# Kernel optimization log

Hardware: AMD Instinct MI355X
Metric: run time of the kernel (lower is better)

Reference implementation:

```python
import jax, jax.numpy as jnp
import numpy as np

T_Q, T_K, B, H, V = 32, 48, 64, 1024, 32320
MASK_FILL = -65504.0  # GNMT uses fp16 min


def setup_inputs() -> dict:
    key = jax.random.key(0)
    ks = jax.random.split(key, 12)
    s = 0.02
    inp = {
        "input1": jax.random.normal(ks[0], (T_K, B, H), jnp.float32),
        "input0": jax.random.normal(ks[1], (T_K, B, H), jnp.float32),
        "input2": jax.random.randint(ks[2], (B,), 1, T_K + 1),          # context lengths in [1, T_K]
        "input3": jax.random.randint(ks[3], (T_Q, B), 0, V),            # decoder token ids
        "emb": (jax.random.normal(ks[4], (V, H), jnp.float32) * 0.1).at[0].set(0.0),  # padding_idx=0
        "W_ih": jax.random.normal(ks[5], (4 * H, H), jnp.float32) * s,
        "W_hh": jax.random.normal(ks[6], (4 * H, H), jnp.float32) * s,
        "b_ih": jnp.zeros((4 * H,), jnp.float32),
        "b_hh": jnp.zeros((4 * H,), jnp.float32),
        "W_q": jax.random.normal(ks[7], (H, H), jnp.float32) * s,
        "W_k": jax.random.normal(ks[8], (H, H), jnp.float32) * s,
        "v_att": jax.random.normal(ks[9], (H,), jnp.float32) * s,
        "norm_scalar": jnp.array([1.0 / np.sqrt(H)], jnp.float32),
        "norm_bias": jnp.zeros((H,), jnp.float32),
    }
    return inp


def _lstm(x, W_ih, W_hh, b_ih, b_hh):
    # x: (T, B, In). PyTorch LSTM gate order: i, f, g, o. Zero initial state.
    xp = jnp.einsum('tbi,gi->tbg', x, W_ih) + b_ih + b_hh  # (T, B, 4H)
    Hh = W_hh.shape[1]

    def step(carry, xt):
        h, c = carry
        gates = xt + h @ W_hh.T
        i, f, g, o = jnp.split(gates, 4, axis=-1)
        c = jax.nn.sigmoid(f) * c + jax.nn.sigmoid(i) * jnp.tanh(g)
        h = jax.nn.sigmoid(o) * jnp.tanh(c)
        return (h, c), h

    h0 = jnp.zeros((x.shape[1], Hh), x.dtype)
    _, hs = jax.lax.scan(step, (h0, h0), xp)
    return hs  # (T, B, H)


def _forward(input1, input0, input2, input3, emb, W_ih, W_hh, b_ih, b_hh,
             W_q, W_k, v_att, norm_scalar, norm_bias):
    x = emb[input3]                       # (T_Q, B, H) embedding lookup
    ctx = input0 + input1                 # (T_K, B, H) residual-summed encoder context
    rnn_out = _lstm(x, W_ih, W_hh, b_ih, b_hh)   # (T_Q, B, H)

    # Bahdanau attention (batch_first=False -> transpose to batch-first)
    q = rnn_out.transpose(1, 0, 2)        # (B, T_Q, H)
    keys = ctx.transpose(1, 0, 2)         # (B, T_K, H)
    aq = q @ W_q.T                        # (B, T_Q, H)
    ak = keys @ W_k.T                     # (B, T_K, H)
    v = v_att / jnp.linalg.norm(v_att) * norm_scalar[0]  # normalized attention vector
    sum_qk = aq[:, :, None, :] + ak[:, None, :, :] + norm_bias  # (B, T_Q, T_K, H)
    scores = jnp.einsum('bqkh,h->bqk', jnp.tanh(sum_qk), v)
    pad = jnp.arange(T_K)[None, :] >= input2[:, None]            # (B, T_K), True = pad
    scores = jnp.where(pad[:, None, :], MASK_FILL, scores)
    attn = jax.nn.softmax(scores, axis=-1)
    context = jnp.einsum('bqk,bkh->bqh', attn, keys).transpose(1, 0, 2)  # (T_Q, B, H)
    # dropout p=0 -> identity; returns (rnn_outputs, attn_context) = (out12, out11)
    return rnn_out, context


def reference(input1, input0, input2, input3, emb, W_ih, W_hh, b_ih, b_hh,
              W_q, W_k, v_att, norm_scalar, norm_bias):
    return _forward(input1, input0, input2, input3, emb, W_ih, W_hh, b_ih, b_hh,
                    W_q, W_k, v_att, norm_scalar, norm_bias)
```

## Files before the change

kernel.cpp:

```cpp
#include <hip/hip_runtime.h>
#include <hip/hip_bf16.h>

typedef unsigned short u16;
typedef __attribute__((ext_vector_type(8))) short bf16x8;
typedef __attribute__((ext_vector_type(8))) unsigned short us8;
typedef __attribute__((ext_vector_type(4))) float f32x4;

#define T_Q 32
#define T_K 48
#define NB 64
#define HDIM 1024
#define MASK_FILL -65504.0f
#define LSTM_BLOCKS 64

__device__ __forceinline__ float bf2f(u16 v){
  union { unsigned u; float f; } x; x.u = ((unsigned)v) << 16; return x.f;
}
__device__ __forceinline__ u16 f2bf(float f){
  union { float f; unsigned u; } x; x.f = f;
  return (u16)((x.u + 0x7FFFu + ((x.u >> 16) & 1u)) >> 16);
}
__device__ __forceinline__ float sigm(float x){
  return __builtin_amdgcn_rcpf(1.f + __expf(-x));
}
__device__ __forceinline__ float tanh_f(float x){
  float e = __expf(2.f * x);
  return fmaf(-2.f, __builtin_amdgcn_rcpf(e + 1.f), 1.f);
}

__device__ __forceinline__ void st_b32_cc(u16* a, unsigned v){
  asm volatile("global_store_dword %0, %1, off sc0 sc1" :: "v"(a), "v"(v) : "memory");
}
__device__ __forceinline__ void st_flag(int* a, int v){
  asm volatile("global_store_dword %0, %1, off sc0 sc1" :: "v"(a), "v"(v) : "memory");
}
__device__ __forceinline__ int ld_flag(const int* a){
  int r;
  asm volatile("global_load_dword %0, %1, off sc0 sc1\n\ts_waitcnt vmcnt(0)"
               : "=v"(r) : "v"(a) : "memory");
  return r;
}

#define MFMA16(A,B,C) __builtin_amdgcn_mfma_f32_16x16x32_bf16(A,B,C,0,0,0)


__global__ void conv_f2b(const float* __restrict__ s, u16* __restrict__ d){
  size_t i = ((size_t)blockIdx.x * 256 + threadIdx.x) * 4;
  float4 v = *(const float4*)(s + i);
  ushort4 o; o.x = f2bf(v.x); o.y = f2bf(v.y); o.z = f2bf(v.z); o.w = f2bf(v.w);
  *(ushort4*)(d + i) = o;
}

__global__ void gather_x(const int* __restrict__ tok, const float* __restrict__ emb,
                         u16* __restrict__ x){
  int r = blockIdx.x;
  int token = tok[r];
  float4 v = ((const float4*)(emb + (size_t)token * HDIM))[threadIdx.x];
  ushort4 o; o.x = f2bf(v.x); o.y = f2bf(v.y); o.z = f2bf(v.z); o.w = f2bf(v.w);
  ((ushort4*)(x + (size_t)r * HDIM))[threadIdx.x] = o;
}

__global__ void make_keys(const float* __restrict__ a, const float* __restrict__ b,
                          u16* __restrict__ o){
  size_t i = ((size_t)blockIdx.x * 256 + threadIdx.x) * 4;
  float4 va = *(const float4*)(a + i);
  float4 vb = *(const float4*)(b + i);
  ushort4 vo;
  vo.x = f2bf(va.x + vb.x);
  vo.y = f2bf(va.y + vb.y);
  vo.z = f2bf(va.z + vb.z);
  vo.w = f2bf(va.w + vb.w);
  *(ushort4*)(o + i) = vo;
}

__global__ void prep_small(const float* __restrict__ vatt, const float* __restrict__ ns,
                           const float* __restrict__ nb,
                           float* __restrict__ vhat, float* __restrict__ nbias){
  __shared__ float wred[4];
  int t = threadIdx.x, lane = t & 63, w = t >> 6;
  float vv[4]; float s = 0.f;
  #pragma unroll
  for (int j = 0; j < 4; j++){ vv[j] = vatt[t*4 + j]; s += vv[j]*vv[j]; }
  #pragma unroll
  for (int m = 32; m >= 1; m >>= 1) s += __shfl_xor(s, m);
  if (lane == 0) wred[w] = s;
  __syncthreads();
  float tot = wred[0] + wred[1] + wred[2] + wred[3];
  float scale = ns[0] / sqrtf(tot);
  #pragma unroll
  for (int j = 0; j < 4; j++) vhat[t*4 + j] = vv[j] * scale;
  #pragma unroll
  for (int j = 0; j < 4; j++){ int i = t + 256*j; nbias[i] = nb[i]; }
}

__global__ void prep_bsum(const float* __restrict__ bih, const float* __restrict__ bhh,
                          float* __restrict__ bias_sum){
  int i = blockIdx.x * 256 + threadIdx.x;
  bias_sum[i] = bih[i] + bhh[i];
}


template<int OB>
__global__ __launch_bounds__(256) void gemm_bf16(
  const u16* __restrict__ A, const u16* __restrict__ W,
  const float* __restrict__ bias, void* __restrict__ Cv,
  int M, int N, int K)
{
  __shared__ __align__(16) u16 As[4][66][8];
  __shared__ __align__(16) u16 Bs[4][66][8];
  const int t = threadIdx.x;
  const int m0 = blockIdx.y * 64, n0 = blockIdx.x * 64;
  const int lane = t & 63, w = t >> 6;
  const int wm = (w >> 1) * 32, wn = (w & 1) * 32;
  const int lr = lane & 15, g = lane >> 4;
  const int lrow = t >> 2, lkc = t & 3;
  f32x4 acc00 = {0,0,0,0}, acc01 = {0,0,0,0}, acc10 = {0,0,0,0}, acc11 = {0,0,0,0};
  const u16* aptr = A + (size_t)(m0 + lrow) * K + lkc * 8;
  const u16* wptr = W + (size_t)(n0 + lrow) * K + lkc * 8;
  for (int k0 = 0; k0 < K; k0 += 32){
    *(bf16x8*)(&As[lkc][lrow][0]) = *(const bf16x8*)(aptr + k0);
    *(bf16x8*)(&Bs[lkc][lrow][0]) = *(const bf16x8*)(wptr + k0);
    __syncthreads();
    bf16x8 a0 = *(const bf16x8*)(&As[g][wm      + lr][0]);
    bf16x8 a1 = *(const bf16x8*)(&As[g][wm + 16 + lr][0]);
    bf16x8 b0 = *(const bf16x8*)(&Bs[g][wn      + lr][0]);
    bf16x8 b1 = *(const bf16x8*)(&Bs[g][wn + 16 + lr][0]);
    acc00 = MFMA16(a0, b0, acc00);
    acc01 = MFMA16(a0, b1, acc01);
    acc10 = MFMA16(a1, b0, acc10);
    acc11 = MFMA16(a1, b1, acc11);
    __syncthreads();
  }
  const int rb = m0 + wm + g * 4;
  const int cb = n0 + wn + lr;
  float bv0 = bias ? bias[cb]      : 0.f;
  float bv1 = bias ? bias[cb + 16] : 0.f;
  #pragma unroll
  for (int r = 0; r < 4; r++){
    float v00 = acc00[r] + bv0, v01 = acc01[r] + bv1;
    float v10 = acc10[r] + bv0, v11 = acc11[r] + bv1;
    if (OB){
      u16* C = (u16*)Cv;
      C[(size_t)(rb + r)      * N + cb]      = f2bf(v00);
      C[(size_t)(rb + r)      * N + cb + 16] = f2bf(v01);
      C[(size_t)(rb + 16 + r) * N + cb]      = f2bf(v10);
      C[(size_t)(rb + 16 + r) * N + cb + 16] = f2bf(v11);
    } else {
      float* C = (float*)Cv;
      C[(size_t)(rb + r)      * N + cb]      = v00;
      C[(size_t)(rb + r)      * N + cb + 16] = v01;
      C[(size_t)(rb + 16 + r) * N + cb]      = v10;
      C[(size_t)(rb + 16 + r) * N + cb + 16] = v11;
    }
  }
}


__global__ __launch_bounds__(512, 1) void lstm_persistent(
  const float* __restrict__ Whh, const u16* __restrict__ xp,
  u16* __restrict__ hsteps,
  u16* __restrict__ qbuf, float* __restrict__ out0,
  int* __restrict__ flags)
{
  extern __shared__ char smem[];
  u16*  wlds = (u16*)smem;
  float* gl  = (float*)(smem + 131072);

  const int tid = threadIdx.x;
  const int c0 = blockIdx.x * 16;
  const int lane = tid & 63, w = tid >> 6;
  const int gate = w & 3, msub = w >> 2;
  const int lr = lane & 15, g = lane >> 4;

  #pragma unroll
  for (int i = 0; i < 16; i++){
    int e = (i * 512 + tid) * 8;
    int R = e >> 10, k = e & 1023;
    int gg = R >> 4, rr = R & 15, tt = k >> 5, kk = k & 31;
    const float* src = Whh + (size_t)((gg << 10) + c0 + rr) * 1024 + k;
    float4 v0 = *(const float4*)(src);
    float4 v1 = *(const float4*)(src + 4);
    u16* dst = wlds + (((gg * 32 + tt) * 16 + rr) * 32 + kk);
    ushort4 o0, o1;
    o0.x = f2bf(v0.x); o0.y = f2bf(v0.y); o0.z = f2bf(v0.z); o0.w = f2bf(v0.w);
    o1.x = f2bf(v1.x); o1.y = f2bf(v1.y); o1.z = f2bf(v1.z); o1.w = f2bf(v1.w);
    *(ushort4*)dst = o0; *(ushort4*)(dst + 4) = o1;
  }
  __syncthreads();

  const int pb = (tid * 2) >> 4;
  const int pc = (tid * 2) & 15;
  float c_state0 = 0.f, c_state1 = 0.f;

  const int arow = msub * 32 + lr;
  const int jc = g >> 1;
  const int cc = (g & 1) * 8;

  #pragma unroll 1
  for (int step = 0; step < T_Q; step++){
    f32x4 acc0 = {0,0,0,0}, acc1 = {0,0,0,0};

    if (step > 0){
      if (w == 0){
        const int* fp = flags + lane * 16;
        for (;;){
          int f = ld_flag(fp);
          if (__ballot(f >= step) == ~0ull) break;
          __builtin_amdgcn_s_sleep(1);
        }
      }
      __syncthreads();

      const u16* hb = hsteps + (size_t)(step - 1) * 65536;
      const u16* pa0 = hb + (size_t)jc * 1024 + (size_t)arow * 16 + cc;
      const u16* pa1 = pa0 + 16 * 16;
      bf16x8 a0[8], a1[8];
      #pragma unroll
      for (int p = 0; p < 8; p++){
        a0[p] = *(const bf16x8*)(pa0 + p * 2048);
        a1[p] = *(const bf16x8*)(pa1 + p * 2048);
      }
      #pragma unroll
      for (int t = 0; t < 32; t++){
        bf16x8 bfr = *(const bf16x8*)(wlds + ((size_t)(gate * 32 + t) * 16 + lr) * 32 + g * 8);
        acc0 = MFMA16(a0[t & 7], bfr, acc0);
        acc1 = MFMA16(a1[t & 7], bfr, acc1);
        if (t < 24){
          a0[t & 7] = *(const bf16x8*)(pa0 + (t + 8) * 2048);
          a1[t & 7] = *(const bf16x8*)(pa1 + (t + 8) * 2048);
        }
      }
    }

    const u16* xr = xp + ((size_t)(step * NB + pb)) * 4096 + c0 + pc;
    unsigned xw0 = *(const unsigned*)(xr);
    unsigned xw1 = *(const unsigned*)(xr + 1024);
    unsigned xw2 = *(const unsigned*)(xr + 2048);
    unsigned xw3 = *(const unsigned*)(xr + 3072);

    #pragma unroll
    for (int r = 0; r < 4; r++){
      gl[(gate * 64 + msub * 32 +      g * 4 + r) * 16 + lr] = acc0[r];
      gl[(gate * 64 + msub * 32 + 16 + g * 4 + r) * 16 + lr] = acc1[r];
    }
    __syncthreads();

    float hout0, hout1; u16 hb0, hb1;
    {
      float ig = gl[(0 * 64 + pb) * 16 + pc] + bf2f((u16)(xw0 & 0xFFFF));
      float fg = gl[(1 * 64 + pb) * 16 + pc] + bf2f((u16)(xw1 & 0xFFFF));
      float gg = gl[(2 * 64 + pb) * 16 + pc] + bf2f((u16)(xw2 & 0xFFFF));
      float og = gl[(3 * 64 + pb) * 16 + pc] + bf2f((u16)(xw3 & 0xFFFF));
      float cn = sigm(fg) * c_state0 + sigm(ig) * tanh_f(gg);
      c_state0 = cn;
      hout0 = sigm(og) * tanh_f(cn); hb0 = f2bf(hout0);
    }
    {
      float ig = gl[(0 * 64 + pb) * 16 + pc + 1] + bf2f((u16)(xw0 >> 16));
      float fg = gl[(1 * 64 + pb) * 16 + pc + 1] + bf2f((u16)(xw1 >> 16));
      float gg = gl[(2 * 64 + pb) * 16 + pc + 1] + bf2f((u16)(xw2 >> 16));
      float og = gl[(3 * 64 + pb) * 16 + pc + 1] + bf2f((u16)(xw3 >> 16));
      float cn = sigm(fg) * c_state1 + sigm(ig) * tanh_f(gg);
      c_state1 = cn;
      hout1 = sigm(og) * tanh_f(cn); hb1 = f2bf(hout1);
    }

    if (step < T_Q - 1){
      u16* hw = hsteps + (size_t)step * 65536 + (size_t)blockIdx.x * 1024 + pb * 16 + pc;
      unsigned hpack = (unsigned)hb0 | ((unsigned)hb1 << 16);
      st_b32_cc(hw, hpack);
      asm volatile("s_waitcnt vmcnt(0)" ::: "memory");
      __syncthreads();
      if (tid == 0) st_flag(flags + blockIdx.x * 16, step + 1);
    }

    ushort2 hh; hh.x = hb0; hh.y = hb1;
    *(ushort2*)(qbuf + ((size_t)pb * T_Q + step) * HDIM + c0 + pc) = hh;
    float2 ho; ho.x = hout0; ho.y = hout1;
    *(float2*)(out0 + ((size_t)(step * NB + pb)) * HDIM + c0 + pc) = ho;
  }
}


__global__ __launch_bounds__(256) void attn_fused(
  const float* __restrict__ aq, const u16* __restrict__ ak,
  const float* __restrict__ vhat, const u16* __restrict__ keys,
  const int* __restrict__ lens, float* __restrict__ out1)
{
  int b = blockIdx.x >> 5, q = blockIdx.x & 31;
  int t = threadIdx.x, lane = t & 63, w = t >> 6;
  __shared__ float sc[T_K];
  __shared__ float ps[T_K];
  int len = lens[b];
  float aqr[16], vh[16];
  const float* aqp = aq + (size_t)(b * T_Q + q) * HDIM + lane * 16;
  const float* vp  = vhat + lane * 16;
  #pragma unroll
  for (int j = 0; j < 4; j++){
    float4 v0 = ((const float4*)aqp)[j];
    float4 v1 = ((const float4*)vp)[j];
    aqr[j*4+0] = v0.x; aqr[j*4+1] = v0.y; aqr[j*4+2] = v0.z; aqr[j*4+3] = v0.w;
    vh[j*4+0]  = v1.x; vh[j*4+1]  = v1.y; vh[j*4+2]  = v1.z; vh[j*4+3]  = v1.w;
  }

  int kmax = len - w * 12; if (kmax > 12) kmax = 12;
  for (int kk = 0; kk < kmax; kk++){
    int k = w * 12 + kk;
    const u16* akp = ak + (size_t)(k * NB + b) * HDIM + lane * 16;
    us8 a0 = *(const us8*)(akp);
    us8 a1 = *(const us8*)(akp + 8);
    float p = 0.f;
    #pragma unroll
    for (int j = 0; j < 8; j++){
      p += tanh_f(aqr[j]     + bf2f(a0[j])) * vh[j];
      p += tanh_f(aqr[8 + j] + bf2f(a1[j])) * vh[8 + j];
    }
    #pragma unroll
    for (int m = 32; m >= 1; m >>= 1) p += __shfl_xor(p, m);
    if (lane == 0) sc[k] = p;
  }
  __syncthreads();
  float mx = -3.0e38f;
  for (int k = 0; k < len; k++) mx = fmaxf(mx, sc[k]);
  if (t < len) ps[t] = __expf(sc[t] - mx);
  __syncthreads();
  float den = 0.f;
  for (int k = 0; k < len; k++) den += ps[k];
  float rden = __builtin_amdgcn_rcpf(den);

  float c0 = 0.f, c1 = 0.f, c2 = 0.f, c3 = 0.f;
  for (int k = 0; k < len; k++){
    float pk = ps[k];
    ushort4 kv = *(const ushort4*)(keys + (size_t)(k * NB + b) * HDIM + t * 4);
    c0 += pk * bf2f(kv.x); c1 += pk * bf2f(kv.y);
    c2 += pk * bf2f(kv.z); c3 += pk * bf2f(kv.w);
  }
  size_t o = (size_t)(q * NB + b) * HDIM + t * 4;
  out1[o + 0] = c0 * rden;
  out1[o + 1] = c1 * rden;
  out1[o + 2] = c2 * rden;
  out1[o + 3] = c3 * rden;
}


extern "C" void kernel_launch(void* const* d_in, const int* in_sizes, int n_in,
                              void* d_out, int out_size, void* d_ws, size_t ws_size,
                              hipStream_t stream)
{
  const float* in1  = (const float*)d_in[0];
  const float* in0  = (const float*)d_in[1];
  const int*   lens = (const int*)d_in[2];
  const int*   toks = (const int*)d_in[3];
  const float* emb  = (const float*)d_in[4];
  const float* Wih  = (const float*)d_in[5];
  const float* Whh  = (const float*)d_in[6];
  const float* bih  = (const float*)d_in[7];
  const float* bhh  = (const float*)d_in[8];
  const float* Wq   = (const float*)d_in[9];
  const float* Wk   = (const float*)d_in[10];
  const float* vatt = (const float*)d_in[11];
  const float* ns   = (const float*)d_in[12];
  const float* nbb  = (const float*)d_in[13];

  char* p = (char*)d_ws;
  u16* x_bf    = (u16*)p;   p += (size_t)2048 * 1024 * 2;
  u16* keys_bf = (u16*)p;   p += (size_t)3072 * 1024 * 2;
  u16* hsteps  = (u16*)p;   p += (size_t)32 * 65536 * 2;
  u16* qbuf    = (u16*)p;   p += (size_t)2048 * 1024 * 2;
  u16* xp      = (u16*)p;   p += (size_t)2048 * 4096 * 2;
  float* vhat  = (float*)p; p += 1024 * 4;
  float* bsum  = (float*)p; p += 4096 * 4;
  float* nbf   = (float*)p; p += 1024 * 4;
  int* flags   = (int*)p;   p += 4096;
  u16* ak      = (u16*)p;   p += (size_t)3072 * 1024 * 2;
  u16* Wih_bf  = (u16*)p;   p += (size_t)4096 * 1024 * 2;
  u16* Wq_bf   = (u16*)p;   p += (size_t)1024 * 1024 * 2;
  u16* Wk_bf   = (u16*)p;   p += (size_t)1024 * 1024 * 2;
  float* aq    = (float*)xp;

  float* out0 = (float*)d_out;
  float* out1 = out0 + (size_t)T_Q * NB * HDIM;

  hipMemsetAsync(flags, 0, 4096, stream);

  conv_f2b<<<4096, 256, 0, stream>>>(Wih, Wih_bf);
  conv_f2b<<<1024, 256, 0, stream>>>(Wq,  Wq_bf);
  conv_f2b<<<1024, 256, 0, stream>>>(Wk,  Wk_bf);
  gather_x<<<2048, 256, 0, stream>>>(toks, emb, x_bf);
  make_keys<<<3072, 256, 0, stream>>>(in1, in0, keys_bf);
  prep_small<<<1, 256, 0, stream>>>(vatt, ns, nbb, vhat, nbf);
  prep_bsum<<<16, 256, 0, stream>>>(bih, bhh, bsum);

  gemm_bf16<1><<<dim3(64, 32), 256, 0, stream>>>(x_bf, Wih_bf, bsum, xp, 2048, 4096, 1024);
  gemm_bf16<1><<<dim3(16, 48), 256, 0, stream>>>(keys_bf, Wk_bf, nbf, ak, 3072, 1024, 1024);

  lstm_persistent<<<LSTM_BLOCKS, 512, 147456, stream>>>(Whh, xp, hsteps, qbuf, out0, flags);

  gemm_bf16<0><<<dim3(16, 32), 256, 0, stream>>>(qbuf, Wq_bf, nullptr, aq, 2048, 1024, 1024);

  attn_fused<<<2048, 256, 0, stream>>>(aq, ak, vhat, keys_bf, lens, out1);
}
```

Measured before the change: 337.8 us.

## Warp-specialize LSTM step: producer waves stage h into LDS, consumer waves run MFMA

The persistent LSTM kernel now splits its 8 waves into 4 producer waves that copy the previous hidden state from global memory into a double-buffered, swizzled LDS stage, and 4 consumer waves that each compute two gates with MFMA from that stage. Before, every wave loaded its A fragments straight from global memory. The change aims to cut redundant global reads and overlap loads with matrix math. In exchange it adds eight block-wide barriers per step, halves the number of MFMA waves, and raises LDS use to 160KB.

New measurement: 465.9 us. +37.9%, slower.

```diff
diff --git a/kernel.cpp b/kernel.cpp
--- a/kernel.cpp
+++ b/kernel.cpp
@@ -163,14 +163,18 @@
   int* __restrict__ flags)
 {
   extern __shared__ char smem[];
-  u16*  wlds = (u16*)smem;
-  float* gl  = (float*)(smem + 131072);
+  u16*  wlds  = (u16*)smem;
+  u16*  stage = (u16*)(smem + 131072);
+  float* gl   = (float*)(smem + 131072);
 
   const int tid = threadIdx.x;
   const int c0 = blockIdx.x * 16;
   const int lane = tid & 63, w = tid >> 6;
-  const int gate = w & 3, msub = w >> 2;
   const int lr = lane & 15, g = lane >> 4;
+  const int gp   = w & 1;
+  const int msub = (w >> 1) & 1;
+  const int g0 = gp * 2, g1q = gp * 2 + 1;
+  const int sid = tid - 256;
 
   #pragma unroll
   for (int i = 0; i < 16; i++){
@@ -192,16 +196,54 @@
   const int pc = (tid * 2) & 15;
   float c_state0 = 0.f, c_state1 = 0.f;
 
-  const int arow = msub * 32 + lr;
   const int jc = g >> 1;
   const int cc = (g & 1) * 8;
+  const int rowbase = (msub * 32 + lr) * 16;
+  const int swzkey = ((lr >> 2) & 3) << 3;
+
+#define STAGE_LOAD(regs, chunk) \
+  do { const uint4* src_ = (const uint4*)(hb + (chunk) * 8192 + sid * 32); \
+       regs[0] = src_[0]; regs[1] = src_[1]; regs[2] = src_[2]; regs[3] = src_[3]; } while (0)
+
+#define STAGE_WRITE(regs, chunk) \
+  do { u16* dstb_ = stage + (((chunk) & 1) * 8192); \
+       _Pragma("unroll") \
+       for (int p_ = 0; p_ < 4; p_++){ \
+         int idx_ = sid * 32 + p_ * 8; \
+         int phys_ = idx_ ^ (((idx_ >> 6) & 3) << 3); \
+         *(uint4*)(dstb_ + phys_) = regs[p_]; \
+       } } while (0)
+
+#define SEGC(kk) \
+  do { const u16* buf_ = stage + (((kk) & 1) * 8192); \
+       _Pragma("unroll") \
+       for (int t_ = 0; t_ < 4; t_++){ \
+         int idx0_ = (t_ * 2 + jc) * 1024 + rowbase + cc; \
+         bf16x8 a0_ = *(const bf16x8*)(buf_ + (idx0_ ^ swzkey)); \
+         bf16x8 a1_ = *(const bf16x8*)(buf_ + ((idx0_ + 256) ^ swzkey)); \
+         const u16* wb0_ = wlds + ((size_t)(g0  * 32 + (kk) * 4 + t_) * 16 + lr) * 32 + g * 8; \
+         const u16* wb1_ = wlds + ((size_t)(g1q * 32 + (kk) * 4 + t_) * 16 + lr) * 32 + g * 8; \
+         bf16x8 b0_ = *(const bf16x8*)(wb0_); \
+         bf16x8 b1_ = *(const bf16x8*)(wb1_); \
+         accA0 = MFMA16(a0_, b0_, accA0); accA1 = MFMA16(a1_, b0_, accA1); \
+         accB0 = MFMA16(a0_, b1_, accB0); accB1 = MFMA16(a1_, b1_, accB1); \
+       } } while (0)
 
   #pragma unroll 1
   for (int step = 0; step < T_Q; step++){
-    f32x4 acc0 = {0,0,0,0}, acc1 = {0,0,0,0};
+    const u16* xr = xp + ((size_t)(step * NB + pb)) * 4096 + c0 + pc;
+    unsigned xw0 = *(const unsigned*)(xr);
+    unsigned xw1 = *(const unsigned*)(xr + 1024);
+    unsigned xw2 = *(const unsigned*)(xr + 2048);
+    unsigned xw3 = *(const unsigned*)(xr + 3072);
+
+    f32x4 accA0 = {0,0,0,0}, accA1 = {0,0,0,0};
+    f32x4 accB0 = {0,0,0,0}, accB1 = {0,0,0,0};
 
     if (step > 0){
-      if (w == 0){
+      const u16* hb = hsteps + (size_t)(step - 1) * 65536;
+
+      if (w == 4){
         const int* fp = flags + lane * 16;
         for (;;){
           int f = ld_flag(fp);
@@ -211,37 +253,40 @@
       }
       __syncthreads();
 
-      const u16* hb = hsteps + (size_t)(step - 1) * 65536;
-      const u16* pa0 = hb + (size_t)jc * 1024 + (size_t)arow * 16 + cc;
-      const u16* pa1 = pa0 + 16 * 16;
-      bf16x8 a0[8], a1[8];
+      uint4 rA[4], rB[4];
+      if (w >= 4){
+        STAGE_LOAD(rA, 0);
+        STAGE_WRITE(rA, 0);
+        STAGE_LOAD(rB, 1);
+      }
+      __syncthreads();
+
+      if (w < 4) SEGC(0); else { STAGE_WRITE(rB, 1); STAGE_LOAD(rA, 2); }
+      __syncthreads();
+      if (w < 4) SEGC(1); else { STAGE_WRITE(rA, 2); STAGE_LOAD(rB, 3); }
+      __syncthreads();
+      if (w < 4) SEGC(2); else { STAGE_WRITE(rB, 3); STAGE_LOAD(rA, 4); }
+      __syncthreads();
+      if (w < 4) SEGC(3); else { STAGE_WRITE(rA, 4); STAGE_LOAD(rB, 5); }
+      __syncthreads();
+      if (w < 4) SEGC(4); else { STAGE_WRITE(rB, 5); STAGE_LOAD(rA, 6); }
+      __syncthreads();
+      if (w < 4) SEGC(5); else { STAGE_WRITE(rA, 6); STAGE_LOAD(rB, 7); }
+      __syncthreads();
+      if (w < 4) SEGC(6); else { STAGE_WRITE(rB, 7); }
+      __syncthreads();
+      if (w < 4) SEGC(7);
+      __syncthreads();
+    }
+
+    if (w < 4){
       #pragma unroll
-      for (int p = 0; p < 8; p++){
-        a0[p] = *(const bf16x8*)(pa0 + p * 2048);
-        a1[p] = *(const bf16x8*)(pa1 + p * 2048);
+      for (int r = 0; r < 4; r++){
+        gl[(g0  * 64 + msub * 32 +      g * 4 + r) * 16 + lr] = accA0[r];
+        gl[(g0  * 64 + msub * 32 + 16 + g * 4 + r) * 16 + lr] = accA1[r];
+        gl[(g1q * 64 + msub * 32 +      g * 4 + r) * 16 + lr] = accB0[r];
+        gl[(g1q * 64 + msub * 32 + 16 + g * 4 + r) * 16 + lr] = accB1[r];
       }
-      #pragma unroll
-      for (int t = 0; t < 32; t++){
-        bf16x8 bfr = *(const bf16x8*)(wlds + ((size_t)(gate * 32 + t) * 16 + lr) * 32 + g * 8);
-        acc0 = MFMA16(a0[t & 7], bfr, acc0);
-        acc1 = MFMA16(a1[t & 7], bfr, acc1);
-        if (t < 24){
-          a0[t & 7] = *(const bf16x8*)(pa0 + (t + 8) * 2048);
-          a1[t & 7] = *(const bf16x8*)(pa1 + (t + 8) * 2048);
-        }
-      }
-    }
-
-    const u16* xr = xp + ((size_t)(step * NB + pb)) * 4096 + c0 + pc;
-    unsigned xw0 = *(const unsigned*)(xr);
-    unsigned xw1 = *(const unsigned*)(xr + 1024);
-    unsigned xw2 = *(const unsigned*)(xr + 2048);
-    unsigned xw3 = *(const unsigned*)(xr + 3072);
-
-    #pragma unroll
-    for (int r = 0; r < 4; r++){
-      gl[(gate * 64 + msub * 32 +      g * 4 + r) * 16 + lr] = acc0[r];
-      gl[(gate * 64 + msub * 32 + 16 + g * 4 + r) * 16 + lr] = acc1[r];
     }
     __syncthreads();
 
@@ -279,6 +324,9 @@
     float2 ho; ho.x = hout0; ho.y = hout1;
     *(float2*)(out0 + ((size_t)(step * NB + pb)) * HDIM + c0 + pc) = ho;
   }
+#undef STAGE_LOAD
+#undef STAGE_WRITE
+#undef SEGC
 }
 
 
@@ -394,7 +442,7 @@
   gemm_bf16<1><<<dim3(64, 32), 256, 0, stream>>>(x_bf, Wih_bf, bsum, xp, 2048, 4096, 1024);
   gemm_bf16<1><<<dim3(16, 48), 256, 0, stream>>>(keys_bf, Wk_bf, nbf, ak, 3072, 1024, 1024);
 
-  lstm_persistent<<<LSTM_BLOCKS, 512, 147456, stream>>>(Whh, xp, hsteps, qbuf, out0, flags);
+  lstm_persistent<<<LSTM_BLOCKS, 512, 163840, stream>>>(Whh, xp, hsteps, qbuf, out0, flags);
 
   gemm_bf16<0><<<dim3(16, 32), 256, 0, stream>>>(qbuf, Wq_bf, nullptr, aq, 2048, 1024, 1024);
 
```

## Split LSTM batch into two halves with separate flags to overlap grid sync

Applied to the files above, without the earlier changes.

The persistent LSTM kernel now handles the 64-row batch as two independent 32-row halves, each with its own hidden-state buffer and flag array. Each step runs the two halves back to back, so one half's cross-block wait and flag exchange can overlap with the other half's MFMA work. The intent is to hide the grid-wide synchronisation latency of the recurrent dependency. The cost is twice as many barriers and flag polls per step, and only half the threads doing the elementwise gate math in each phase.

Measured after the change: 368.0 us. 1.09x slower.

```diff
diff --git a/kernel.cpp b/kernel.cpp
--- a/kernel.cpp
+++ b/kernel.cpp
@@ -158,9 +158,9 @@
 
 __global__ __launch_bounds__(512, 1) void lstm_persistent(
   const float* __restrict__ Whh, const u16* __restrict__ xp,
-  u16* __restrict__ hsteps,
+  u16* __restrict__ hsA, u16* __restrict__ hsB,
   u16* __restrict__ qbuf, float* __restrict__ out0,
-  int* __restrict__ flags)
+  int* __restrict__ flagsA, int* __restrict__ flagsB)
 {
   extern __shared__ char smem[];
   u16*  wlds = (u16*)smem;
@@ -188,21 +188,22 @@
   }
   __syncthreads();
 
-  const int pb = (tid * 2) >> 4;
-  const int pc = (tid * 2) & 15;
-  float c_state0 = 0.f, c_state1 = 0.f;
-
-  const int arow = msub * 32 + lr;
+  const int pb2 = tid >> 3;
+  const int pc  = (tid * 2) & 15;
+  float cA0 = 0.f, cA1 = 0.f, cB0 = 0.f, cB1 = 0.f;
+
+  const int arow2 = msub * 16 + lr;
   const int jc = g >> 1;
   const int cc = (g & 1) * 8;
 
-  #pragma unroll 1
-  for (int step = 0; step < T_Q; step++){
-    f32x4 acc0 = {0,0,0,0}, acc1 = {0,0,0,0};
-
+  int step = 0;
+
+  auto phase = [&](u16* hs, int* fl, const unsigned* xw, float& cs0, float& cs1,
+                   int rowoff) __attribute__((always_inline)) {
+    f32x4 acc_e = {0,0,0,0}, acc_o = {0,0,0,0};
     if (step > 0){
       if (w == 0){
-        const int* fp = flags + lane * 16;
+        const int* fp = fl + lane * 16;
         for (;;){
           int f = ld_flag(fp);
           if (__ballot(f >= step) == ~0ull) break;
@@ -211,73 +212,75 @@
       }
       __syncthreads();
 
-      const u16* hb = hsteps + (size_t)(step - 1) * 65536;
-      const u16* pa0 = hb + (size_t)jc * 1024 + (size_t)arow * 16 + cc;
-      const u16* pa1 = pa0 + 16 * 16;
-      bf16x8 a0[8], a1[8];
+      const u16* hb = hs + (size_t)(step - 1) * 32768;
+      const u16* pa = hb + (size_t)jc * 512 + (size_t)arow2 * 16 + cc;
+      bf16x8 a[8];
       #pragma unroll
-      for (int p = 0; p < 8; p++){
-        a0[p] = *(const bf16x8*)(pa0 + p * 2048);
-        a1[p] = *(const bf16x8*)(pa1 + p * 2048);
-      }
+      for (int p = 0; p < 8; p++) a[p] = *(const bf16x8*)(pa + p * 1024);
       #pragma unroll
       for (int t = 0; t < 32; t++){
         bf16x8 bfr = *(const bf16x8*)(wlds + ((size_t)(gate * 32 + t) * 16 + lr) * 32 + g * 8);
-        acc0 = MFMA16(a0[t & 7], bfr, acc0);
-        acc1 = MFMA16(a1[t & 7], bfr, acc1);
-        if (t < 24){
-          a0[t & 7] = *(const bf16x8*)(pa0 + (t + 8) * 2048);
-          a1[t & 7] = *(const bf16x8*)(pa1 + (t + 8) * 2048);
-        }
+        if (t & 1) acc_o = MFMA16(a[t & 7], bfr, acc_o);
+        else       acc_e = MFMA16(a[t & 7], bfr, acc_e);
+        if (t < 24) a[t & 7] = *(const bf16x8*)(pa + (t + 8) * 1024);
       }
     }
-
-    const u16* xr = xp + ((size_t)(step * NB + pb)) * 4096 + c0 + pc;
-    unsigned xw0 = *(const unsigned*)(xr);
-    unsigned xw1 = *(const unsigned*)(xr + 1024);
-    unsigned xw2 = *(const unsigned*)(xr + 2048);
-    unsigned xw3 = *(const unsigned*)(xr + 3072);
-
     #pragma unroll
-    for (int r = 0; r < 4; r++){
-      gl[(gate * 64 + msub * 32 +      g * 4 + r) * 16 + lr] = acc0[r];
-      gl[(gate * 64 + msub * 32 + 16 + g * 4 + r) * 16 + lr] = acc1[r];
-    }
+    for (int r = 0; r < 4; r++)
+      gl[(gate * 32 + msub * 16 + g * 4 + r) * 16 + lr] = acc_e[r] + acc_o[r];
     __syncthreads();
 
-    float hout0, hout1; u16 hb0, hb1;
-    {
-      float ig = gl[(0 * 64 + pb) * 16 + pc] + bf2f((u16)(xw0 & 0xFFFF));
-      float fg = gl[(1 * 64 + pb) * 16 + pc] + bf2f((u16)(xw1 & 0xFFFF));
-      float gg = gl[(2 * 64 + pb) * 16 + pc] + bf2f((u16)(xw2 & 0xFFFF));
-      float og = gl[(3 * 64 + pb) * 16 + pc] + bf2f((u16)(xw3 & 0xFFFF));
-      float cn = sigm(fg) * c_state0 + sigm(ig) * tanh_f(gg);
-      c_state0 = cn;
-      hout0 = sigm(og) * tanh_f(cn); hb0 = f2bf(hout0);
-    }
-    {
-      float ig = gl[(0 * 64 + pb) * 16 + pc + 1] + bf2f((u16)(xw0 >> 16));
-      float fg = gl[(1 * 64 + pb) * 16 + pc + 1] + bf2f((u16)(xw1 >> 16));
-      float gg = gl[(2 * 64 + pb) * 16 + pc + 1] + bf2f((u16)(xw2 >> 16));
-      float og = gl[(3 * 64 + pb) * 16 + pc + 1] + bf2f((u16)(xw3 >> 16));
-      float cn = sigm(fg) * c_state1 + sigm(ig) * tanh_f(gg);
-      c_state1 = cn;
-      hout1 = sigm(og) * tanh_f(cn); hb1 = f2bf(hout1);
+    u16 hb0 = 0, hb1 = 0; float ho0 = 0.f, ho1 = 0.f;
+    if (tid < 256){
+      float ig0 = gl[(0 * 32 + pb2) * 16 + pc] + bf2f((u16)(xw[0] & 0xFFFF));
+      float fg0 = gl[(1 * 32 + pb2) * 16 + pc] + bf2f((u16)(xw[1] & 0xFFFF));
+      float gg0 = gl[(2 * 32 + pb2) * 16 + pc] + bf2f((u16)(xw[2] & 0xFFFF));
+      float og0 = gl[(3 * 32 + pb2) * 16 + pc] + bf2f((u16)(xw[3] & 0xFFFF));
+      float cn0 = sigm(fg0) * cs0 + sigm(ig0) * tanh_f(gg0);
+      cs0 = cn0; ho0 = sigm(og0) * tanh_f(cn0); hb0 = f2bf(ho0);
+      float ig1 = gl[(0 * 32 + pb2) * 16 + pc + 1] + bf2f((u16)(xw[0] >> 16));
+      float fg1 = gl[(1 * 32 + pb2) * 16 + pc + 1] + bf2f((u16)(xw[1] >> 16));
+      float gg1 = gl[(2 * 32 + pb2) * 16 + pc + 1] + bf2f((u16)(xw[2] >> 16));
+      float og1 = gl[(3 * 32 + pb2) * 16 + pc + 1] + bf2f((u16)(xw[3] >> 16));
+      float cn1 = sigm(fg1) * cs1 + sigm(ig1) * tanh_f(gg1);
+      cs1 = cn1; ho1 = sigm(og1) * tanh_f(cn1); hb1 = f2bf(ho1);
     }
 
     if (step < T_Q - 1){
-      u16* hw = hsteps + (size_t)step * 65536 + (size_t)blockIdx.x * 1024 + pb * 16 + pc;
-      unsigned hpack = (unsigned)hb0 | ((unsigned)hb1 << 16);
-      st_b32_cc(hw, hpack);
+      if (tid < 256){
+        u16* hw = hs + (size_t)step * 32768 + (size_t)blockIdx.x * 512 + pb2 * 16 + pc;
+        st_b32_cc(hw, (unsigned)hb0 | ((unsigned)hb1 << 16));
+      }
       asm volatile("s_waitcnt vmcnt(0)" ::: "memory");
       __syncthreads();
-      if (tid == 0) st_flag(flags + blockIdx.x * 16, step + 1);
-    }
-
-    ushort2 hh; hh.x = hb0; hh.y = hb1;
-    *(ushort2*)(qbuf + ((size_t)pb * T_Q + step) * HDIM + c0 + pc) = hh;
-    float2 ho; ho.x = hout0; ho.y = hout1;
-    *(float2*)(out0 + ((size_t)(step * NB + pb)) * HDIM + c0 + pc) = ho;
+      if (tid == 0) st_flag(fl + blockIdx.x * 16, step + 1);
+    } else {
+      __syncthreads();
+    }
+
+    if (tid < 256){
+      int brow = rowoff + pb2;
+      ushort2 hh; hh.x = hb0; hh.y = hb1;
+      *(ushort2*)(qbuf + ((size_t)brow * T_Q + step) * HDIM + c0 + pc) = hh;
+      float2 ho; ho.x = ho0; ho.y = ho1;
+      *(float2*)(out0 + ((size_t)(step * NB + brow)) * HDIM + c0 + pc) = ho;
+    }
+  };
+
+  #pragma unroll 1
+  for (step = 0; step < T_Q; step++){
+    unsigned xwA[4] = {0,0,0,0}, xwB[4] = {0,0,0,0};
+    if (tid < 256){
+      const u16* xrA = xp + ((size_t)(step * NB + pb2)) * 4096 + c0 + pc;
+      const u16* xrB = xrA + (size_t)32 * 4096;
+      #pragma unroll
+      for (int j = 0; j < 4; j++){
+        xwA[j] = *(const unsigned*)(xrA + j * 1024);
+        xwB[j] = *(const unsigned*)(xrB + j * 1024);
+      }
+    }
+    phase(hsA, flagsA, xwA, cA0, cA1, 0);
+    phase(hsB, flagsB, xwB, cB0, cB1, 32);
   }
 }
 
@@ -365,13 +368,15 @@
   char* p = (char*)d_ws;
   u16* x_bf    = (u16*)p;   p += (size_t)2048 * 1024 * 2;
   u16* keys_bf = (u16*)p;   p += (size_t)3072 * 1024 * 2;
-  u16* hsteps  = (u16*)p;   p += (size_t)32 * 65536 * 2;
+  u16* hsA     = (u16*)p;   p += (size_t)32 * 32768 * 2;
+  u16* hsB     = (u16*)p;   p += (size_t)32 * 32768 * 2;
   u16* qbuf    = (u16*)p;   p += (size_t)2048 * 1024 * 2;
   u16* xp      = (u16*)p;   p += (size_t)2048 * 4096 * 2;
   float* vhat  = (float*)p; p += 1024 * 4;
   float* bsum  = (float*)p; p += 4096 * 4;
   float* nbf   = (float*)p; p += 1024 * 4;
-  int* flags   = (int*)p;   p += 4096;
+  int* flagsA  = (int*)p;   p += 4096;
+  int* flagsB  = (int*)p;   p += 4096;
   u16* ak      = (u16*)p;   p += (size_t)3072 * 1024 * 2;
   u16* Wih_bf  = (u16*)p;   p += (size_t)4096 * 1024 * 2;
   u16* Wq_bf   = (u16*)p;   p += (size_t)1024 * 1024 * 2;
@@ -381,7 +386,7 @@
   float* out0 = (float*)d_out;
   float* out1 = out0 + (size_t)T_Q * NB * HDIM;
 
-  hipMemsetAsync(flags, 0, 4096, stream);
+  hipMemsetAsync(flagsA, 0, 8192, stream);
 
   conv_f2b<<<4096, 256, 0, stream>>>(Wih, Wih_bf);
   conv_f2b<<<1024, 256, 0, stream>>>(Wq,  Wq_bf);
@@ -394,7 +399,8 @@
   gemm_bf16<1><<<dim3(64, 32), 256, 0, stream>>>(x_bf, Wih_bf, bsum, xp, 2048, 4096, 1024);
   gemm_bf16<1><<<dim3(16, 48), 256, 0, stream>>>(keys_bf, Wk_bf, nbf, ak, 3072, 1024, 1024);
 
-  lstm_persistent<<<LSTM_BLOCKS, 512, 147456, stream>>>(Whh, xp, hsteps, qbuf, out0, flags);
+  lstm_persistent<<<LSTM_BLOCKS, 512, 139264, stream>>>(Whh, xp, hsA, hsB,
+                                                        qbuf, out0, flagsA, flagsB);
 
   gemm_bf16<0><<<dim3(16, 32), 256, 0, stream>>>(qbuf, Wq_bf, nullptr, aq, 2048, 1024, 1024);
 
```
